# Performance work log

Hardware: AMD Instinct MI355X
Metric: run time of the kernel (lower is better)

## Reference

```python
import jax, jax.numpy as jnp
import numpy as np

D_MODEL = 1024
NUM_HEADS = 16
D_K = D_MODEL // NUM_HEADS
B, S = 2, 2048


def setup_inputs() -> dict:
    key = jax.random.key(0)
    ks = jax.random.split(key, 11)
    scale = 1.0 / np.sqrt(D_MODEL)
    inp = {
        "q": jax.random.normal(ks[0], (B, S, D_MODEL), dtype=jnp.float32),
        "k": jax.random.normal(ks[1], (B, S, D_MODEL), dtype=jnp.float32),
        "v": jax.random.normal(ks[2], (B, S, D_MODEL), dtype=jnp.float32),
        "w_q": jax.random.normal(ks[3], (D_MODEL, D_MODEL), dtype=jnp.float32) * scale,
        "b_q": jnp.zeros((D_MODEL,), dtype=jnp.float32),
        "w_k": jax.random.normal(ks[4], (D_MODEL, D_MODEL), dtype=jnp.float32) * scale,
        "b_k": jnp.zeros((D_MODEL,), dtype=jnp.float32),
        "w_v": jax.random.normal(ks[5], (D_MODEL, D_MODEL), dtype=jnp.float32) * scale,
        "b_v": jnp.zeros((D_MODEL,), dtype=jnp.float32),
        "w_o": jax.random.normal(ks[6], (D_MODEL, D_MODEL), dtype=jnp.float32) * scale,
        "b_o": jnp.zeros((D_MODEL,), dtype=jnp.float32),
    }
    return inp


def reference(q, k, v, w_q, b_q, w_k, b_k, w_v, b_v, w_o, b_o):
    # Linear projections (torch Linear: x @ W^T + b)
    def proj(x, w, b):
        # [B,S,D] -> [B,H,S,d_k]
        y = x @ w.T + b
        return y.reshape(B, S, NUM_HEADS, D_K).transpose(0, 2, 1, 3)

    query = proj(q, w_q, b_q)
    key_ = proj(k, w_k, b_k)
    value = proj(v, w_v, b_v)

    # scores: [B,H,S,S]
    scores = jnp.einsum('bhqd,bhkd->bhqk', query, key_) / jnp.sqrt(
        jnp.asarray(D_K, dtype=query.dtype))
    attn = jax.nn.softmax(scores, axis=-1)
    x = jnp.einsum('bhqk,bhkd->bhqd', attn, value)
    x = x.transpose(0, 2, 1, 3).reshape(B, S, D_MODEL)
    return x @ w_o.T + b_o
```

## Files before the change

### kernel.cpp

```cpp
#include <hip/hip_runtime.h>
#include <stdint.h>

#define D_MODEL 1024
#define NHEAD 16
#define DK 64
#define BATCH 2
#define SEQ 2048
#define MROWS (BATCH * SEQ)
#define KVB 128
#define NIT (SEQ / KVB)
#define QSCALE 0.18033688011112042f

typedef __attribute__((ext_vector_type(8))) __bf16 bf16x8;
typedef __attribute__((ext_vector_type(2))) __bf16 bf16x2;
typedef __attribute__((ext_vector_type(4))) float f32x4;
typedef __attribute__((ext_vector_type(4))) unsigned int u32x4;
typedef __attribute__((ext_vector_type(2))) unsigned int u32x2;

#if defined(__has_builtin)
#if __has_builtin(__builtin_amdgcn_permlane32_swap) && \
    __has_builtin(__builtin_amdgcn_permlane16_swap)
#define HAVE_PERMLANE_SWAP 1
#endif
#endif
#ifndef HAVE_PERMLANE_SWAP
#define HAVE_PERMLANE_SWAP 0
#endif

__device__ __forceinline__ float exp2_hw(float x) {
  return __builtin_amdgcn_exp2f(x);
}

__device__ __forceinline__ f32x4 f4zero() {
  f32x4 z = {0.f, 0.f, 0.f, 0.f};
  return z;
}

__device__ __forceinline__ f32x4 mfma_bf16(bf16x8 a, bf16x8 b, f32x4 c) {
  return __builtin_amdgcn_mfma_f32_16x16x32_bf16(a, b, c, 0, 0, 0);
}

__device__ __forceinline__ void gload_lds16(const void* g, void* l) {
  __builtin_amdgcn_global_load_lds(
      (const __attribute__((address_space(1))) unsigned int*)g,
      (__attribute__((address_space(3))) unsigned int*)l, 16, 0, 0);
}

__device__ __forceinline__ unsigned short f2b(float x) {
  unsigned int u = __float_as_uint(x);
  u += 0x7fffu + ((u >> 16) & 1u);
  return (unsigned short)(u >> 16);
}

#if HAVE_PERMLANE_SWAP
__device__ __forceinline__ u32x2 pl32(unsigned int a, unsigned int b) {
  return __builtin_amdgcn_permlane32_swap(a, b, false, false);
}
__device__ __forceinline__ u32x2 pl16(unsigned int a, unsigned int b) {
  return __builtin_amdgcn_permlane16_swap(a, b, false, false);
}
#endif

__global__ void cvt_all_kernel(const float* __restrict__ q, const float* __restrict__ k,
                               const float* __restrict__ v, const float* __restrict__ wq,
                               const float* __restrict__ wk, const float* __restrict__ wv,
                               const float* __restrict__ wo,
                               unsigned short* __restrict__ actout,
                               unsigned short* __restrict__ wout) {
  const size_t SZA = (size_t)MROWS * D_MODEL;
  const size_t SZW = (size_t)D_MODEL * D_MODEL;
  const int bid = blockIdx.x;
  const float* in;
  unsigned short* out;
  int i;
  if (bid < 12288) {
    const int seg = bid >> 12, ib = bid & 4095;
    in = seg == 0 ? q : seg == 1 ? k : v;
    out = actout + (size_t)seg * SZA;
    i = ib * 256 + threadIdx.x;
  } else {
    const int b2 = bid - 12288;
    const int seg = b2 >> 10, ib = b2 & 1023;
    in = seg == 0 ? wq : seg == 1 ? wk : seg == 2 ? wv : wo;
    out = wout + (size_t)seg * SZW;
    i = ib * 256 + threadIdx.x;
  }
  float4 x = ((const float4*)in)[i];
  ushort4 r;
  r.x = f2b(x.x); r.y = f2b(x.y); r.z = f2b(x.z); r.w = f2b(x.w);
  ((ushort4*)out)[i] = r;
}

template <int EPI, int BROW>
__device__ __forceinline__ void gemm_body128(const unsigned short* __restrict__ A,
                                             const unsigned short* __restrict__ B,
                                             const float* __restrict__ bias,
                                             float scale,
                                             unsigned short* __restrict__ outb,
                                             float* __restrict__ outf, int bx,
                                             int M, int N, int K,
                                             unsigned short* sA, unsigned short* sB) {
  const int tid = threadIdx.x;
  const int w = tid >> 6, l = tid & 63;
  const int nTN = N >> 7;
  const int bm = bx / nTN, bn = bx % nTN;
  const int rowBase = bm << 7, colBase = bn << 7;
  const int wm = w >> 1, wn = w & 1;
  const int g = l >> 4, c16 = l & 15;

  f32x4 acc[4][4];
#pragma unroll
  for (int i = 0; i < 4; i++)
#pragma unroll
    for (int j = 0; j < 4; j++) acc[i][j] = f4zero();

  const int rloc = l >> 2;
  const int uch = (l & 3) ^ (rloc & 3);

  for (int kk = 0; kk < K; kk += 32) {
    __syncthreads();
#pragma unroll
    for (int h = 0; h < 2; h++) {
      const int r0 = w * 16 + h * 64;
      gload_lds16(A + (size_t)(rowBase + r0 + rloc) * K + kk + uch * 8,
                  &sA[r0 * 32]);
      gload_lds16(B + (size_t)(colBase + r0 + rloc) * K + kk + uch * 8,
                  &sB[r0 * 32]);
    }
    __syncthreads();

    bf16x8 af[4], bfr[4];
#pragma unroll
    for (int mt = 0; mt < 4; mt++) {
      const int r = wm * 64 + mt * 16 + c16;
      af[mt] = *(const bf16x8*)&sA[r * 32 + (g ^ (r & 3)) * 8];
    }
#pragma unroll
    for (int nt = 0; nt < 4; nt++) {
      const int r = wn * 64 + nt * 16 + c16;
      bfr[nt] = *(const bf16x8*)&sB[r * 32 + (g ^ (r & 3)) * 8];
    }
#pragma unroll
    for (int mt = 0; mt < 4; mt++)
#pragma unroll
      for (int nt = 0; nt < 4; nt++)
        acc[mt][nt] = mfma_bf16(af[mt], bfr[nt], acc[mt][nt]);
  }

#pragma unroll
  for (int mt = 0; mt < 4; mt++) {
    float brow[4];
    if (BROW) {
#pragma unroll
      for (int i = 0; i < 4; i++)
        brow[i] = bias[rowBase + wm * 64 + mt * 16 + g * 4 + i];
    }
#pragma unroll
    for (int nt = 0; nt < 4; nt++) {
      const int col = colBase + wn * 64 + nt * 16 + c16;
      const float bcol = BROW ? 0.f : bias[col];
#pragma unroll
      for (int i = 0; i < 4; i++) {
        const int row = rowBase + wm * 64 + mt * 16 + g * 4 + i;
        const float bv = BROW ? brow[i] : bcol;
        const float v = (acc[mt][nt][i] + bv) * scale;
        if (EPI == 0)
          outb[(size_t)row * N + col] = f2b(v);
        else
          outf[(size_t)row * N + col] = v;
      }
    }
  }
}

__device__ __forceinline__ void gemm_body64(const unsigned short* __restrict__ A,
                                            const unsigned short* __restrict__ B,
                                            const float* __restrict__ bias,
                                            float* __restrict__ outf, int bx,
                                            int M, int N, int K,
                                            unsigned short* sA, unsigned short* sB) {
  const int tid = threadIdx.x;
  const int w = tid >> 6, l = tid & 63;
  const int nTN = N >> 6;
  const int bm = bx / nTN, bn = bx % nTN;
  const int rowBase = bm << 7, colBase = bn << 6;
  const int g = l >> 4, c16 = l & 15;

  f32x4 acc[2][4];
#pragma unroll
  for (int i = 0; i < 2; i++)
#pragma unroll
    for (int j = 0; j < 4; j++) acc[i][j] = f4zero();

  const int rloc = l >> 2;
  const int uch = (l & 3) ^ (rloc & 3);

  for (int kk = 0; kk < K; kk += 32) {
    __syncthreads();
    gload_lds16(A + (size_t)(rowBase + w * 16 + rloc) * K + kk + uch * 8,
                &sA[(w * 16) * 32]);
    gload_lds16(A + (size_t)(rowBase + 64 + w * 16 + rloc) * K + kk + uch * 8,
                &sA[(64 + w * 16) * 32]);
    gload_lds16(B + (size_t)(colBase + w * 16 + rloc) * K + kk + uch * 8,
                &sB[(w * 16) * 32]);
    __syncthreads();

    bf16x8 af[2], bfr[4];
#pragma unroll
    for (int mt = 0; mt < 2; mt++) {
      const int r = w * 32 + mt * 16 + c16;
      af[mt] = *(const bf16x8*)&sA[r * 32 + (g ^ (r & 3)) * 8];
    }
#pragma unroll
    for (int nt = 0; nt < 4; nt++) {
      const int r = nt * 16 + c16;
      bfr[nt] = *(const bf16x8*)&sB[r * 32 + (g ^ (r & 3)) * 8];
    }
#pragma unroll
    for (int mt = 0; mt < 2; mt++)
#pragma unroll
      for (int nt = 0; nt < 4; nt++)
        acc[mt][nt] = mfma_bf16(af[mt], bfr[nt], acc[mt][nt]);
  }

#pragma unroll
  for (int mt = 0; mt < 2; mt++)
#pragma unroll
    for (int nt = 0; nt < 4; nt++) {
      const int col = colBase + nt * 16 + c16;
      const float bv = bias[col];
#pragma unroll
      for (int i = 0; i < 4; i++) {
        const int row = rowBase + w * 32 + mt * 16 + g * 4 + i;
        outf[(size_t)row * N + col] = acc[mt][nt][i] + bv;
      }
    }
}

__global__ __launch_bounds__(256, 3) void gemm_qkv_kernel(
    const unsigned short* __restrict__ Abase, const unsigned short* __restrict__ Wbase,
    const float* __restrict__ bq, const float* __restrict__ bk,
    const float* __restrict__ bv, unsigned short* __restrict__ QKout,
    unsigned short* __restrict__ VTout) {
  __shared__ __attribute__((aligned(16))) unsigned short sA[128 * 32];
  __shared__ __attribute__((aligned(16))) unsigned short sB[128 * 32];
  const int nblk = 256;
  const int gid = blockIdx.x / nblk, bx = blockIdx.x % nblk;
  const size_t SZA = (size_t)MROWS * D_MODEL;
  const size_t SZW = (size_t)D_MODEL * D_MODEL;
  if (gid < 2) {
    const float* bias = gid == 0 ? bq : bk;
    const float scale = gid == 0 ? QSCALE : 1.0f;
    gemm_body128<0, 0>(Abase + (size_t)gid * SZA, Wbase + (size_t)gid * SZW, bias,
                       scale, QKout + (size_t)gid * SZA, nullptr, bx, MROWS,
                       D_MODEL, D_MODEL, sA, sB);
  } else {
    gemm_body128<0, 1>(Wbase + 2 * SZW, Abase + 2 * SZA, bv, 1.0f, VTout, nullptr,
                       bx, D_MODEL, MROWS, D_MODEL, sA, sB);
  }
}

__global__ __launch_bounds__(256, 4) void gemm_out_kernel(
    const unsigned short* __restrict__ A, const unsigned short* __restrict__ B,
    const float* __restrict__ bias, float* __restrict__ out) {
  __shared__ __attribute__((aligned(16))) unsigned short sA[128 * 32];
  __shared__ __attribute__((aligned(16))) unsigned short sB[64 * 32];
  gemm_body64(A, B, bias, out, blockIdx.x, MROWS, D_MODEL, D_MODEL, sA, sB);
}

__global__ __launch_bounds__(256, 2) void attn_kernel(
    const unsigned short* __restrict__ Qh, const unsigned short* __restrict__ Kh,
    const unsigned short* __restrict__ Vt, unsigned short* __restrict__ Xh) {
  __shared__ __attribute__((aligned(16))) unsigned short sK[2][2][64 * 64];
  __shared__ __attribute__((aligned(16))) unsigned short sV[2][2][64 * 64];

  const int tid = threadIdx.x, w = tid >> 6, l = tid & 63;
  const int fid = blockIdx.x;
  const int L = (fid & 7) * 64 + (fid >> 3);
  const int bh = L >> 4, qx = L & 15;
  const int b = bh >> 4, h = bh & 15;
  const int q0 = qx * 128 + w * 32;
  const int g = l >> 4, c16 = l & 15;

  bf16x8 qf[2][2];
#pragma unroll
  for (int qs = 0; qs < 2; ++qs)
#pragma unroll
    for (int f = 0; f < 2; ++f)
      qf[qs][f] = *(const bf16x8*)&Qh[(size_t)(b * SEQ + q0 + qs * 16 + c16) * D_MODEL +
                                      h * DK + f * 32 + g * 8];

  const u32x4 onesu = {0x3F803F80u, 0x3F803F80u, 0x3F803F80u, 0x3F803F80u};
  const bf16x8 onesf = __builtin_bit_cast(bf16x8, onesu);

  f32x4 acc[2][4], accl[2];
#pragma unroll
  for (int qs = 0; qs < 2; ++qs) {
#pragma unroll
    for (int dt = 0; dt < 4; ++dt) acc[qs][dt] = f4zero();
    accl[qs] = f4zero();
  }

  const int srow = l >> 3, sch = (l & 7) ^ (srow & 7);

  auto STAGE = [&](int pbuf, int kv0) {
#pragma unroll
    for (int half = 0; half < 2; ++half)
#pragma unroll
      for (int hh = 0; hh < 2; ++hh) {
        const int r0 = w * 16 + hh * 8;
        const int kvh = kv0 + half * 64;
        gload_lds16(
            Kh + (size_t)(b * SEQ + kvh + r0 + srow) * D_MODEL + h * DK + sch * 8,
            &sK[pbuf][half][r0 * 64]);
        gload_lds16(
            Vt + (size_t)(h * DK + r0 + srow) * MROWS + b * SEQ + kvh + sch * 8,
            &sV[pbuf][half][r0 * 64]);
      }
  };

  auto STEPH = [&](const unsigned short* sKp, const unsigned short* sVp) {
    f32x4 st[2][4];
#pragma unroll
    for (int kt = 0; kt < 4; ++kt) {
      bf16x8 kf[2];
#pragma unroll
      for (int f = 0; f < 2; ++f) {
        const int key = kt * 16 + c16;
        const int ch = (f * 4 + g) ^ (key & 7);
        kf[f] = *(const bf16x8*)&sKp[key * 64 + ch * 8];
      }
#pragma unroll
      for (int qs = 0; qs < 2; ++qs) {
        f32x4 s = mfma_bf16(kf[0], qf[qs][0], f4zero());
        st[qs][kt] = mfma_bf16(kf[1], qf[qs][1], s);
      }
    }

    unsigned int Qpk[2][4][2];
#pragma unroll
    for (int qs = 0; qs < 2; ++qs)
#pragma unroll
      for (int kt = 0; kt < 4; ++kt) {
        float pv[4];
#pragma unroll
        for (int i = 0; i < 4; ++i) pv[i] = exp2_hw(st[qs][kt][i]);
#pragma unroll
        for (int hh = 0; hh < 2; ++hh) {
          bf16x2 t2;
          t2.x = (__bf16)pv[hh * 2];
          t2.y = (__bf16)pv[hh * 2 + 1];
          Qpk[qs][kt][hh] = __builtin_bit_cast(unsigned int, t2);
        }
      }

#pragma unroll
    for (int ks = 0; ks < 2; ++ks) {
      bf16x8 pfrag[2];
#pragma unroll
      for (int qs = 0; qs < 2; ++qs) {
        unsigned int pw[4];
#if HAVE_PERMLANE_SWAP
#pragma unroll
        for (int hh = 0; hh < 2; ++hh) {
          u32x2 s1 = pl32(Qpk[qs][2 * ks][hh], Qpk[qs][2 * ks + 1][hh]);
          u32x2 s2 = pl16(s1.x, s1.y);
          pw[hh] = s2.x;
          pw[2 + hh] = s2.y;
        }
#else
#pragma unroll
        for (int hh = 0; hh < 2; ++hh) {
          const unsigned int a = Qpk[qs][2 * ks][hh], bb = Qpk[qs][2 * ks + 1][hh];
          const unsigned int as = __shfl_xor((int)a, 32);
          const unsigned int bs = __shfl_xor((int)bb, 32);
          const unsigned int r0 = (l >= 32) ? bs : a;
          const unsigned int r1 = (l >= 32) ? bb : as;
          const unsigned int t0 = __shfl_xor((int)r0, 16);
          const unsigned int t1 = __shfl_xor((int)r1, 16);
          pw[hh] = (g & 1) ? t1 : r0;
          pw[2 + hh] = (g & 1) ? r1 : t0;
        }
#endif
        u32x4 pv4 = {pw[0], pw[1], pw[2], pw[3]};
        pfrag[qs] = __builtin_bit_cast(bf16x8, pv4);
      }
      __builtin_amdgcn_s_setprio(1);
      accl[0] = mfma_bf16(pfrag[0], onesf, accl[0]);
      accl[1] = mfma_bf16(pfrag[1], onesf, accl[1]);
#pragma unroll
      for (int dt = 0; dt < 4; ++dt) {
        const int d = dt * 16 + c16;
        const int ch = (ks * 4 + g) ^ (d & 7);
        bf16x8 vfrag = *(const bf16x8*)&sVp[d * 64 + ch * 8];
        acc[0][dt] = mfma_bf16(pfrag[0], vfrag, acc[0][dt]);
        acc[1][dt] = mfma_bf16(pfrag[1], vfrag, acc[1][dt]);
      }
      __builtin_amdgcn_s_setprio(0);
    }
  };

  STAGE(0, 0);
  __syncthreads();

  for (int it = 0; it < NIT; it += 2) {
    if (it + 1 < NIT) STAGE(1, (it + 1) * KVB);
    STEPH(&sK[0][0][0], &sV[0][0][0]);
    STEPH(&sK[0][1][0], &sV[0][1][0]);
    __syncthreads();
    if (it + 2 < NIT) STAGE(0, (it + 2) * KVB);
    STEPH(&sK[1][0][0], &sV[1][0][0]);
    STEPH(&sK[1][1][0], &sV[1][1][0]);
    __syncthreads();
  }

#pragma unroll
  for (int qs = 0; qs < 2; ++qs) {
    float linv[4];
#pragma unroll
    for (int i = 0; i < 4; ++i) linv[i] = __builtin_amdgcn_rcpf(accl[qs][i]);
#pragma unroll
    for (int dt = 0; dt < 4; ++dt)
#pragma unroll
      for (int i = 0; i < 4; ++i) {
        const int row = b * SEQ + q0 + qs * 16 + g * 4 + i;
        const int col = h * DK + dt * 16 + c16;
        Xh[(size_t)row * D_MODEL + col] = f2b(acc[qs][dt][i] * linv[i]);
      }
  }
}

extern "C" void kernel_launch(void* const* d_in, const int* in_sizes, int n_in,
                              void* d_out, int out_size, void* d_ws, size_t ws_size,
                              hipStream_t stream) {
  (void)in_sizes; (void)n_in; (void)out_size; (void)ws_size;
  const float* q = (const float*)d_in[0];
  const float* k = (const float*)d_in[1];
  const float* v = (const float*)d_in[2];
  const float* w_q = (const float*)d_in[3];
  const float* b_q = (const float*)d_in[4];
  const float* w_k = (const float*)d_in[5];
  const float* b_k = (const float*)d_in[6];
  const float* w_v = (const float*)d_in[7];
  const float* b_v = (const float*)d_in[8];
  const float* w_o = (const float*)d_in[9];
  const float* b_o = (const float*)d_in[10];

  const size_t SZ_ACT = (size_t)MROWS * D_MODEL;
  const size_t SZ_W = (size_t)D_MODEL * D_MODEL;
  char* ws = (char*)d_ws;
  unsigned short* qb = (unsigned short*)(ws);
  unsigned short* Xh = (unsigned short*)(ws);
  unsigned short* Qproj = (unsigned short*)(ws + 6 * SZ_ACT);
  unsigned short* Vt = (unsigned short*)(ws + 10 * SZ_ACT);
  unsigned short* wqb = (unsigned short*)(ws + 12 * SZ_ACT);
  unsigned short* wob = (unsigned short*)(ws + 12 * SZ_ACT + 6 * SZ_W);

  cvt_all_kernel<<<16384, 256, 0, stream>>>(q, k, v, w_q, w_k, w_v, w_o, qb, wqb);

  gemm_qkv_kernel<<<3 * 256, 256, 0, stream>>>(qb, wqb, b_q, b_k, b_v, Qproj, Vt);

  attn_kernel<<<512, 256, 0, stream>>>(Qproj, Qproj + SZ_ACT, Vt, Xh);

  gemm_out_kernel<<<512, 256, 0, stream>>>(Xh, wob, b_o, (float*)d_out);
}
```

Baseline: 117.1 us.

## Fuse fp32-to-bf16 activation conversion into QKV GEMM tile loads

```diff
diff --git a/kernel.cpp b/kernel.cpp
--- a/kernel.cpp
+++ b/kernel.cpp
@@ -61,49 +61,31 @@
 }
 #endif
 
-__global__ void cvt_all_kernel(const float* __restrict__ q, const float* __restrict__ k,
-                               const float* __restrict__ v, const float* __restrict__ wq,
-                               const float* __restrict__ wk, const float* __restrict__ wv,
-                               const float* __restrict__ wo,
-                               unsigned short* __restrict__ actout,
-                               unsigned short* __restrict__ wout) {
-  const size_t SZA = (size_t)MROWS * D_MODEL;
+__global__ void cvt_w_kernel(const float* __restrict__ wq, const float* __restrict__ wk,
+                             const float* __restrict__ wv, const float* __restrict__ wo,
+                             unsigned short* __restrict__ wout) {
   const size_t SZW = (size_t)D_MODEL * D_MODEL;
   const int bid = blockIdx.x;
-  const float* in;
-  unsigned short* out;
-  int i;
-  if (bid < 12288) {
-    const int seg = bid >> 12, ib = bid & 4095;
-    in = seg == 0 ? q : seg == 1 ? k : v;
-    out = actout + (size_t)seg * SZA;
-    i = ib * 256 + threadIdx.x;
-  } else {
-    const int b2 = bid - 12288;
-    const int seg = b2 >> 10, ib = b2 & 1023;
-    in = seg == 0 ? wq : seg == 1 ? wk : seg == 2 ? wv : wo;
-    out = wout + (size_t)seg * SZW;
-    i = ib * 256 + threadIdx.x;
-  }
+  const int seg = bid >> 10, ib = bid & 1023;
+  const float* in = seg == 0 ? wq : seg == 1 ? wk : seg == 2 ? wv : wo;
+  unsigned short* out = wout + (size_t)seg * SZW;
+  const int i = ib * 256 + threadIdx.x;
   float4 x = ((const float4*)in)[i];
   ushort4 r;
   r.x = f2b(x.x); r.y = f2b(x.y); r.z = f2b(x.z); r.w = f2b(x.w);
   ((ushort4*)out)[i] = r;
 }
 
-template <int EPI, int BROW>
-__device__ __forceinline__ void gemm_body128(const unsigned short* __restrict__ A,
-                                             const unsigned short* __restrict__ B,
+template <int AF32, int BF32, int BROW>
+__device__ __forceinline__ void gemm_body128(const void* __restrict__ Aptr,
+                                             const void* __restrict__ Bptr,
                                              const float* __restrict__ bias,
                                              float scale,
                                              unsigned short* __restrict__ outb,
-                                             float* __restrict__ outf, int bx,
-                                             int M, int N, int K,
+                                             int bm, int bn, int M, int N, int K,
                                              unsigned short* sA, unsigned short* sB) {
   const int tid = threadIdx.x;
   const int w = tid >> 6, l = tid & 63;
-  const int nTN = N >> 7;
-  const int bm = bx / nTN, bn = bx % nTN;
   const int rowBase = bm << 7, colBase = bn << 7;
   const int wm = w >> 1, wn = w & 1;
   const int g = l >> 4, c16 = l & 15;
@@ -116,16 +98,55 @@
 
   const int rloc = l >> 2;
   const int uch = (l & 3) ^ (rloc & 3);
+  const int rt = tid >> 1, hhf = tid & 1;
 
   for (int kk = 0; kk < K; kk += 32) {
     __syncthreads();
-#pragma unroll
-    for (int h = 0; h < 2; h++) {
-      const int r0 = w * 16 + h * 64;
-      gload_lds16(A + (size_t)(rowBase + r0 + rloc) * K + kk + uch * 8,
-                  &sA[r0 * 32]);
-      gload_lds16(B + (size_t)(colBase + r0 + rloc) * K + kk + uch * 8,
-                  &sB[r0 * 32]);
+    if (AF32) {
+      const float* Af = (const float*)Aptr;
+      const size_t base = (size_t)(rowBase + rt) * K + kk + hhf * 16;
+      float4 f0 = *(const float4*)&Af[base];
+      float4 f1 = *(const float4*)&Af[base + 4];
+      float4 f2 = *(const float4*)&Af[base + 8];
+      float4 f3 = *(const float4*)&Af[base + 12];
+      bf16x8 r0, r1;
+      r0[0] = (__bf16)f0.x; r0[1] = (__bf16)f0.y; r0[2] = (__bf16)f0.z; r0[3] = (__bf16)f0.w;
+      r0[4] = (__bf16)f1.x; r0[5] = (__bf16)f1.y; r0[6] = (__bf16)f1.z; r0[7] = (__bf16)f1.w;
+      r1[0] = (__bf16)f2.x; r1[1] = (__bf16)f2.y; r1[2] = (__bf16)f2.z; r1[3] = (__bf16)f2.w;
+      r1[4] = (__bf16)f3.x; r1[5] = (__bf16)f3.y; r1[6] = (__bf16)f3.z; r1[7] = (__bf16)f3.w;
+      *(bf16x8*)&sA[rt * 32 + ((hhf * 2 + 0) ^ (rt & 3)) * 8] = r0;
+      *(bf16x8*)&sA[rt * 32 + ((hhf * 2 + 1) ^ (rt & 3)) * 8] = r1;
+    } else {
+      const unsigned short* Ab = (const unsigned short*)Aptr;
+#pragma unroll
+      for (int h = 0; h < 2; h++) {
+        const int r0 = w * 16 + h * 64;
+        gload_lds16(Ab + (size_t)(rowBase + r0 + rloc) * K + kk + uch * 8,
+                    &sA[r0 * 32]);
+      }
+    }
+    if (BF32) {
+      const float* Bf = (const float*)Bptr;
+      const size_t base = (size_t)(colBase + rt) * K + kk + hhf * 16;
+      float4 f0 = *(const float4*)&Bf[base];
+      float4 f1 = *(const float4*)&Bf[base + 4];
+      float4 f2 = *(const float4*)&Bf[base + 8];
+      float4 f3 = *(const float4*)&Bf[base + 12];
+      bf16x8 r0, r1;
+      r0[0] = (__bf16)f0.x; r0[1] = (__bf16)f0.y; r0[2] = (__bf16)f0.z; r0[3] = (__bf16)f0.w;
+      r0[4] = (__bf16)f1.x; r0[5] = (__bf16)f1.y; r0[6] = (__bf16)f1.z; r0[7] = (__bf16)f1.w;
+      r1[0] = (__bf16)f2.x; r1[1] = (__bf16)f2.y; r1[2] = (__bf16)f2.z; r1[3] = (__bf16)f2.w;
+      r1[4] = (__bf16)f3.x; r1[5] = (__bf16)f3.y; r1[6] = (__bf16)f3.z; r1[7] = (__bf16)f3.w;
+      *(bf16x8*)&sB[rt * 32 + ((hhf * 2 + 0) ^ (rt & 3)) * 8] = r0;
+      *(bf16x8*)&sB[rt * 32 + ((hhf * 2 + 1) ^ (rt & 3)) * 8] = r1;
+    } else {
+      const unsigned short* Bb = (const unsigned short*)Bptr;
+#pragma unroll
+      for (int h = 0; h < 2; h++) {
+        const int r0 = w * 16 + h * 64;
+        gload_lds16(Bb + (size_t)(colBase + r0 + rloc) * K + kk + uch * 8,
+                    &sB[r0 * 32]);
+      }
     }
     __syncthreads();
 
@@ -163,11 +184,7 @@
       for (int i = 0; i < 4; i++) {
         const int row = rowBase + wm * 64 + mt * 16 + g * 4 + i;
         const float bv = BROW ? brow[i] : bcol;
-        const float v = (acc[mt][nt][i] + bv) * scale;
-        if (EPI == 0)
-          outb[(size_t)row * N + col] = f2b(v);
-        else
-          outf[(size_t)row * N + col] = v;
+        outb[(size_t)row * N + col] = f2b((acc[mt][nt][i] + bv) * scale);
       }
     }
   }
@@ -238,25 +255,29 @@
 }
 
 __global__ __launch_bounds__(256, 3) void gemm_qkv_kernel(
-    const unsigned short* __restrict__ Abase, const unsigned short* __restrict__ Wbase,
+    const float* __restrict__ qin, const float* __restrict__ kin,
+    const float* __restrict__ vin, const unsigned short* __restrict__ Wbase,
     const float* __restrict__ bq, const float* __restrict__ bk,
     const float* __restrict__ bv, unsigned short* __restrict__ QKout,
     unsigned short* __restrict__ VTout) {
   __shared__ __attribute__((aligned(16))) unsigned short sA[128 * 32];
   __shared__ __attribute__((aligned(16))) unsigned short sB[128 * 32];
-  const int nblk = 256;
-  const int gid = blockIdx.x / nblk, bx = blockIdx.x % nblk;
+  const int gid = blockIdx.x >> 8, rb = blockIdx.x & 255;
+  const int c = rb & 7, j = rb >> 3;
   const size_t SZA = (size_t)MROWS * D_MODEL;
   const size_t SZW = (size_t)D_MODEL * D_MODEL;
   if (gid < 2) {
+    const int bm = c * 4 + (j >> 3), bn = j & 7;
+    const float* act = gid == 0 ? qin : kin;
     const float* bias = gid == 0 ? bq : bk;
     const float scale = gid == 0 ? QSCALE : 1.0f;
-    gemm_body128<0, 0>(Abase + (size_t)gid * SZA, Wbase + (size_t)gid * SZW, bias,
-                       scale, QKout + (size_t)gid * SZA, nullptr, bx, MROWS,
-                       D_MODEL, D_MODEL, sA, sB);
+    gemm_body128<1, 0, 0>(act, Wbase + (size_t)gid * SZW, bias, scale,
+                          QKout + (size_t)gid * SZA, bm, bn, MROWS, D_MODEL,
+                          D_MODEL, sA, sB);
   } else {
-    gemm_body128<0, 1>(Wbase + 2 * SZW, Abase + 2 * SZA, bv, 1.0f, VTout, nullptr,
-                       bx, D_MODEL, MROWS, D_MODEL, sA, sB);
+    const int bm = j & 7, bn = c * 4 + (j >> 3);
+    gemm_body128<0, 1, 1>(Wbase + 2 * SZW, vin, bv, 1.0f, VTout, bm, bn,
+                          D_MODEL, MROWS, D_MODEL, sA, sB);
   }
 }
 
@@ -449,16 +470,16 @@
   const size_t SZ_ACT = (size_t)MROWS * D_MODEL;
   const size_t SZ_W = (size_t)D_MODEL * D_MODEL;
   char* ws = (char*)d_ws;
-  unsigned short* qb = (unsigned short*)(ws);
   unsigned short* Xh = (unsigned short*)(ws);
   unsigned short* Qproj = (unsigned short*)(ws + 6 * SZ_ACT);
   unsigned short* Vt = (unsigned short*)(ws + 10 * SZ_ACT);
   unsigned short* wqb = (unsigned short*)(ws + 12 * SZ_ACT);
   unsigned short* wob = (unsigned short*)(ws + 12 * SZ_ACT + 6 * SZ_W);
 
-  cvt_all_kernel<<<16384, 256, 0, stream>>>(q, k, v, w_q, w_k, w_v, w_o, qb, wqb);
-
-  gemm_qkv_kernel<<<3 * 256, 256, 0, stream>>>(qb, wqb, b_q, b_k, b_v, Qproj, Vt);
+  cvt_w_kernel<<<4096, 256, 0, stream>>>(w_q, w_k, w_v, w_o, wqb);
+
+  gemm_qkv_kernel<<<3 * 256, 256, 0, stream>>>(q, k, v, wqb, b_q, b_k, b_v,
+                                               Qproj, Vt);
 
   attn_kernel<<<512, 256, 0, stream>>>(Qproj, Qproj + SZ_ACT, Vt, Xh);
 
```

Result: faster. 114.6 us (-2.1%).
